# Performance work log

Hardware: AMD Instinct MI355X
Metric: run time of the kernel (lower is better)

The kernel has to match this reference:

```python
import jax, jax.numpy as jnp
import numpy as np

B, C_IN, N, K, NUM_CLASS, EMB = 8, 3, 1024, 40, 40, 1024
EPS = 1e-5


def setup_inputs() -> dict:
    key = jax.random.key(0)
    ks = jax.random.split(key, 20)

    def w(k, shape):
        return jax.random.normal(k, shape, jnp.float32) * 0.05

    def bn(k, c):
        k1, k2, k3, k4 = jax.random.split(k, 4)
        g = jax.random.uniform(k1, (c,), jnp.float32, 0.5, 1.5)
        b = jax.random.normal(k2, (c,), jnp.float32) * 0.1
        m = jax.random.normal(k3, (c,), jnp.float32) * 0.1
        v = jax.random.uniform(k4, (c,), jnp.float32, 0.5, 1.5)
        return jnp.stack([g, b, m, v])  # [4, C]

    return {
        "x": jax.random.normal(ks[0], (B, C_IN, N), jnp.float32),
        "w1": w(ks[1], (64, 6)),
        "w2": w(ks[2], (64, 128)),
        "w3": w(ks[3], (128, 128)),
        "w4": w(ks[4], (256, 256)),
        "w5": w(ks[5], (EMB, 512)),
        "l1": w(ks[6], (512, 2 * EMB)),
        "l2w": w(ks[7], (256, 512)),
        "l2b": w(ks[8], (256,)),
        "l3w": w(ks[9], (NUM_CLASS, 256)),
        "l3b": w(ks[10], (NUM_CLASS,)),
        "bn1": bn(ks[11], 64),
        "bn2": bn(ks[12], 64),
        "bn3": bn(ks[13], 128),
        "bn4": bn(ks[14], 256),
        "bn5": bn(ks[15], EMB),
        "bn6": bn(ks[16], 512),
        "bn7": bn(ks[17], 256),
    }


def _bn(x, p, axis):
    # eval-mode batchnorm: p = [gamma, beta, running_mean, running_var]
    shape = [1] * x.ndim
    shape[axis] = p.shape[1]
    g, b, m, v = (p[i].reshape(shape) for i in range(4))
    return (x - m) * g * jax.lax.rsqrt(v + EPS) + b


def _lrelu(x):
    return jnp.where(x >= 0, x, 0.2 * x)


def _knn(x, k):
    # x: [B, C, N] -> neighbor indices [B, N, k] by largest negative sq-distance
    xx = jnp.sum(x * x, axis=1)  # [B, N]
    inner = jnp.einsum('bcn,bcm->bnm', x, x)  # [B, N, N]
    pd = 2.0 * inner - xx[:, :, None] - xx[:, None, :]
    return jax.lax.top_k(pd, k)[1]


def _graph_feature(x, k):
    # x: [B, C, N] -> edge features [B, 2C, N, k] = cat(nbr - center, center)
    idx = _knn(x, k)  # [B, N, k]
    xt = jnp.transpose(x, (0, 2, 1))  # [B, N, C]
    nb = jax.vmap(lambda xt_b, i_b: xt_b[i_b])(xt, idx)  # [B, N, k, C]
    ctr = jnp.broadcast_to(xt[:, :, None, :], nb.shape)
    feat = jnp.concatenate([nb - ctr, ctr], axis=-1)
    return jnp.transpose(feat, (0, 3, 1, 2))


def _edge_conv(x, w, bnp, k):
    f = _graph_feature(x, k)  # [B, 2C, N, k]
    h = jnp.einsum('oc,bcnk->bonk', w, f)  # 1x1 conv2d, no bias
    h = _lrelu(_bn(h, bnp, 1))
    return jnp.max(h, axis=-1)  # max over k neighbors -> [B, O, N]


def reference(x, w1, w2, w3, w4, w5, l1, l2w, l2b, l3w, l3b,
              bn1, bn2, bn3, bn4, bn5, bn6, bn7):
    x1 = _edge_conv(x, w1, bn1, K)   # [B, 64, N]
    x2 = _edge_conv(x1, w2, bn2, K)  # [B, 64, N]
    x3 = _edge_conv(x2, w3, bn3, K)  # [B, 128, N]
    x4 = _edge_conv(x3, w4, bn4, K)  # [B, 256, N]
    xc = jnp.concatenate([x1, x2, x3, x4], axis=1)  # [B, 512, N]
    e = _lrelu(_bn(jnp.einsum('oc,bcn->bon', w5, xc), bn5, 1))  # [B, EMB, N]
    g = jnp.concatenate([jnp.max(e, axis=-1), jnp.mean(e, axis=-1)], axis=1)  # [B, 2*EMB]
    h = _lrelu(_bn(g @ l1.T, bn6, 1))            # linear1 (no bias) + bn6
    h = _lrelu(_bn(h @ l2w.T + l2b, bn7, 1))     # linear2 + bn7 (dropout = eval identity)
    logits = h @ l3w.T + l3b                     # linear3
    return logits, jax.nn.log_softmax(logits, axis=-1)
```

## Files before the change

### kernel.cpp

```cpp
#include <hip/hip_runtime.h>
#include <hip/hip_bf16.h>
#include <math.h>

#define BB 8
#define NN 1024
#define KK 40
#define EMBD 1024
#define EPSF 1e-5f
#define ROWS 8
#define BBNN (BB * NN)

template <int CTRL>
__device__ __forceinline__ unsigned long long dppmax64(unsigned long long cur) {
    unsigned olo = (unsigned)__builtin_amdgcn_update_dpp(0, (int)(unsigned)cur, CTRL, 0xf, 0xf, true);
    unsigned ohi = (unsigned)__builtin_amdgcn_update_dpp(0, (int)(unsigned)(cur >> 32), CTRL, 0xf, 0xf, true);
    unsigned long long o = ((unsigned long long)ohi << 32) | olo;
    return o > cur ? o : cur;
}

__global__ __launch_bounds__(256) void layer_kernel(const float* __restrict__ x, int C, int bstride,
                                                    const float* __restrict__ w, int O,
                                                    int* __restrict__ gidx,
                                                    float* __restrict__ ya, float* __restrict__ yc) {
    extern __shared__ float lds[];
    int tid = threadIdx.x;

    if (blockIdx.x < BB * 128) {
        float* S = lds;
        int b = blockIdx.x >> 7;
        int n0 = (blockIdx.x & 127) * ROWS;
        const float* xb = x + (size_t)b * bstride;

        float acc[ROWS][4];
        float xxa[4] = {0.f, 0.f, 0.f, 0.f};
#pragma unroll
        for (int r = 0; r < ROWS; ++r)
#pragma unroll
            for (int j = 0; j < 4; ++j) acc[r][j] = 0.f;

        for (int c = 0; c < C; ++c) {
            float4 xm  = *(const float4*)&xb[c * NN + (tid << 2)];
            float4 ce0 = *(const float4*)&xb[c * NN + n0];
            float4 ce1 = *(const float4*)&xb[c * NN + n0 + 4];
            xxa[0] = fmaf(xm.x, xm.x, xxa[0]);
            xxa[1] = fmaf(xm.y, xm.y, xxa[1]);
            xxa[2] = fmaf(xm.z, xm.z, xxa[2]);
            xxa[3] = fmaf(xm.w, xm.w, xxa[3]);
            float ce[8] = {ce0.x, ce0.y, ce0.z, ce0.w, ce1.x, ce1.y, ce1.z, ce1.w};
#pragma unroll
            for (int r = 0; r < ROWS; ++r) {
                acc[r][0] = fmaf(ce[r], xm.x, acc[r][0]);
                acc[r][1] = fmaf(ce[r], xm.y, acc[r][1]);
                acc[r][2] = fmaf(ce[r], xm.z, acc[r][2]);
                acc[r][3] = fmaf(ce[r], xm.w, acc[r][3]);
            }
        }
#pragma unroll
        for (int r = 0; r < ROWS; ++r) {
            float4 sv;
            sv.x = 2.f * acc[r][0] - xxa[0];
            sv.y = 2.f * acc[r][1] - xxa[1];
            sv.z = 2.f * acc[r][2] - xxa[2];
            sv.w = 2.f * acc[r][3] - xxa[3];
            *(float4*)&S[r * NN + (tid << 2)] = sv;
        }
        __syncthreads();

        int wave = tid >> 6, lane = tid & 63;
        int ra = wave << 1, rb = ra + 1;
        unsigned long long va[16], vb[16];
#pragma unroll
        for (int j = 0; j < 16; ++j) {
            unsigned ua = __float_as_uint(S[ra * NN + lane + 64 * j]);
            unsigned ub = __float_as_uint(S[rb * NN + lane + 64 * j]);
            ua ^= (unsigned)((int)ua >> 31) | 0x80000000u;
            ub ^= (unsigned)((int)ub >> 31) | 0x80000000u;
            unsigned lo = (unsigned)(1023 - (lane + (j << 6)));
            va[j] = ((unsigned long long)ua << 32) | lo;
            vb[j] = ((unsigned long long)ub << 32) | lo;
        }
#pragma unroll
        for (int k = 2; k <= 16; k <<= 1)
#pragma unroll
        for (int s = k >> 1; s > 0; s >>= 1)
#pragma unroll
        for (int i = 0; i < 16; ++i) {
            int l = i ^ s;
            if (l > i) {
                bool up = ((i & k) == 0);
                { unsigned long long A = va[i], B = va[l];
                  bool sw = up ? (A > B) : (A < B);
                  va[i] = sw ? B : A; va[l] = sw ? A : B; }
                { unsigned long long A = vb[i], B = vb[l];
                  bool sw = up ? (A > B) : (A < B);
                  vb[i] = sw ? B : A; vb[l] = sw ? A : B; }
            }
        }
        int* ga = gidx + (size_t)b * NN + n0 + ra;
        int* gb = gidx + (size_t)b * NN + n0 + rb;
        unsigned long long ha = va[15], hb = vb[15];
        for (int it = 0; it < KK; ++it) {
            unsigned long long ma = ha, mb = hb;
            ma = dppmax64<0x111>(ma); mb = dppmax64<0x111>(mb);
            ma = dppmax64<0x112>(ma); mb = dppmax64<0x112>(mb);
            ma = dppmax64<0x114>(ma); mb = dppmax64<0x114>(mb);
            ma = dppmax64<0x118>(ma); mb = dppmax64<0x118>(mb);
            ma = dppmax64<0x142>(ma); mb = dppmax64<0x142>(mb);
            ma = dppmax64<0x143>(ma); mb = dppmax64<0x143>(mb);
            unsigned wla = (unsigned)__builtin_amdgcn_readlane((int)(unsigned)ma, 63);
            unsigned wha = (unsigned)__builtin_amdgcn_readlane((int)(unsigned)(ma >> 32), 63);
            unsigned wlb = (unsigned)__builtin_amdgcn_readlane((int)(unsigned)mb, 63);
            unsigned whb = (unsigned)__builtin_amdgcn_readlane((int)(unsigned)(mb >> 32), 63);
            if (lane == 0) {
                ga[(size_t)it * BBNN] = 1023 - (int)wla;
                gb[(size_t)it * BBNN] = 1023 - (int)wlb;
            }
            unsigned long long wka = ((unsigned long long)wha << 32) | wla;
            unsigned long long wkb = ((unsigned long long)whb << 32) | wlb;
            bool pa = (ha == wka), pb = (hb == wkb);
#pragma unroll
            for (int j = 15; j > 0; --j) {
                va[j] = pa ? va[j - 1] : va[j];
                vb[j] = pb ? vb[j - 1] : vb[j];
            }
            va[0] = pa ? 0ull : va[0];
            vb[0] = pb ? 0ull : vb[0];
            ha = va[15]; hb = vb[15];
        }
    } else {
        int bid = blockIdx.x - BB * 128;
        float* wls = lds;
        int opb = O >> 3;
        int b  = bid / opb;
        int o0 = (bid % opb) << 3;
        const float* xb = x + (size_t)b * bstride;

        for (int t = tid; t < 8 * C; t += 256) {
            int r = t / C, c = t - r * C;
            float wa = w[(size_t)(o0 + r) * 2 * C + c];
            float wb = w[(size_t)(o0 + r) * 2 * C + C + c];
            wls[t] = wa;
            wls[8 * C + t] = wb - wa;
        }
        __syncthreads();

        float a[8][4], cv[8][4];
#pragma unroll
        for (int r = 0; r < 8; ++r)
#pragma unroll
            for (int j = 0; j < 4; ++j) { a[r][j] = 0.f; cv[r][j] = 0.f; }
        for (int c = 0; c < C; ++c) {
            float4 xm = *(const float4*)&xb[c * NN + (tid << 2)];
#pragma unroll
            for (int r = 0; r < 8; ++r) {
                float wa = wls[r * C + c];
                float wc = wls[8 * C + r * C + c];
                a[r][0]  = fmaf(wa, xm.x, a[r][0]);  cv[r][0] = fmaf(wc, xm.x, cv[r][0]);
                a[r][1]  = fmaf(wa, xm.y, a[r][1]);  cv[r][1] = fmaf(wc, xm.y, cv[r][1]);
                a[r][2]  = fmaf(wa, xm.z, a[r][2]);  cv[r][2] = fmaf(wc, xm.z, cv[r][2]);
                a[r][3]  = fmaf(wa, xm.w, a[r][3]);  cv[r][3] = fmaf(wc, xm.w, cv[r][3]);
            }
        }
#pragma unroll
        for (int r = 0; r < 8; ++r) {
            size_t off = ((size_t)b * O + o0 + r) * NN + (tid << 2);
            *(float4*)&ya[off] = *(float4*)&a[r][0];
            *(float4*)&yc[off] = *(float4*)&cv[r][0];
        }
    }
}

__global__ __launch_bounds__(256) void gmax8_kernel(const float* __restrict__ ya, const float* __restrict__ yc,
                                                    const int* __restrict__ gidx, const float* __restrict__ bnp,
                                                    int O, float* __restrict__ outp, int out_bstride) {
    __shared__ float yrow[8 * NN];
    int tid = threadIdx.x;
    int nt   = blockIdx.x & 3;
    int rest = blockIdx.x >> 2;
    int opb = O >> 3;
    int oc = rest % opb;
    int b  = rest / opb;
    int o0 = oc << 3;
    int n  = (nt << 8) + tid;

    for (int t = tid; t < 8 * NN; t += 256)
        yrow[t] = ya[((size_t)b * O + o0 + (t >> 10)) * NN + (t & 1023)];
    __syncthreads();

    int idx[KK];
    const int* gi = gidx + (size_t)b * NN + n;
#pragma unroll
    for (int k = 0; k < KK; ++k) idx[k] = gi[(size_t)k * BBNN];

#pragma unroll
    for (int r = 0; r < 8; ++r) {
        float m = -INFINITY;
#pragma unroll 8
        for (int k = 0; k < KK; ++k) m = fmaxf(m, yrow[r * NN + idx[k]]);
        m += yc[((size_t)b * O + o0 + r) * NN + n];
        int o = o0 + r;
        float sc = bnp[o] * rsqrtf(bnp[3 * O + o] + EPSF);
        float t0 = (m - bnp[2 * O + o]) * sc + bnp[O + o];
        outp[(size_t)b * out_bstride + (size_t)o * NN + n] = t0 >= 0.f ? t0 : 0.2f * t0;
    }
}

__global__ __launch_bounds__(256) void emb_kernel(const float* __restrict__ xc, const float* __restrict__ w5,
                                                  const float* __restrict__ bnp, float* __restrict__ g) {
    __shared__ float rmax[8][4], rsum[8][4];
    int tid = threadIdx.x;
    int b  = blockIdx.x & 7;
    int o0 = (blockIdx.x >> 3) << 3;
    const float* xcb = xc + (size_t)b * 512 * NN;
    const float* wr  = w5 + (size_t)o0 * 512;

    int n4 = tid << 2;
    float acc[8][4];
#pragma unroll
    for (int r = 0; r < 8; ++r)
#pragma unroll
        for (int j = 0; j < 4; ++j) acc[r][j] = 0.f;

#pragma unroll 2
    for (int c4 = 0; c4 < 128; ++c4) {
        int c = c4 << 2;
        float4 xm0 = *(const float4*)&xcb[(c + 0) * NN + n4];
        float4 xm1 = *(const float4*)&xcb[(c + 1) * NN + n4];
        float4 xm2 = *(const float4*)&xcb[(c + 2) * NN + n4];
        float4 xm3 = *(const float4*)&xcb[(c + 3) * NN + n4];
#pragma unroll
        for (int r = 0; r < 8; ++r) {
            float4 wv = *(const float4*)&wr[r * 512 + c];
            acc[r][0] = fmaf(wv.x, xm0.x, acc[r][0]);
            acc[r][1] = fmaf(wv.x, xm0.y, acc[r][1]);
            acc[r][2] = fmaf(wv.x, xm0.z, acc[r][2]);
            acc[r][3] = fmaf(wv.x, xm0.w, acc[r][3]);
            acc[r][0] = fmaf(wv.y, xm1.x, acc[r][0]);
            acc[r][1] = fmaf(wv.y, xm1.y, acc[r][1]);
            acc[r][2] = fmaf(wv.y, xm1.z, acc[r][2]);
            acc[r][3] = fmaf(wv.y, xm1.w, acc[r][3]);
            acc[r][0] = fmaf(wv.z, xm2.x, acc[r][0]);
            acc[r][1] = fmaf(wv.z, xm2.y, acc[r][1]);
            acc[r][2] = fmaf(wv.z, xm2.z, acc[r][2]);
            acc[r][3] = fmaf(wv.z, xm2.w, acc[r][3]);
            acc[r][0] = fmaf(wv.w, xm3.x, acc[r][0]);
            acc[r][1] = fmaf(wv.w, xm3.y, acc[r][1]);
            acc[r][2] = fmaf(wv.w, xm3.z, acc[r][2]);
            acc[r][3] = fmaf(wv.w, xm3.w, acc[r][3]);
        }
    }

    int lane = tid & 63, wave = tid >> 6;
#pragma unroll
    for (int r = 0; r < 8; ++r) {
        int o = o0 + r;
        float sc = bnp[o] * rsqrtf(bnp[3 * EMBD + o] + EPSF);
        float mu = bnp[2 * EMBD + o], be = bnp[EMBD + o];
        float vmax = -INFINITY, vsum = 0.f;
#pragma unroll
        for (int j = 0; j < 4; ++j) {
            float t0 = (acc[r][j] - mu) * sc + be;
            t0 = t0 >= 0.f ? t0 : 0.2f * t0;
            vmax = fmaxf(vmax, t0);
            vsum += t0;
        }
#pragma unroll
        for (int off = 32; off >= 1; off >>= 1) {
            vmax = fmaxf(vmax, __shfl_xor(vmax, off));
            vsum += __shfl_xor(vsum, off);
        }
        if (lane == 0) { rmax[r][wave] = vmax; rsum[r][wave] = vsum; }
    }
    __syncthreads();
    if (tid < 8) {
        float vm = fmaxf(fmaxf(rmax[tid][0], rmax[tid][1]), fmaxf(rmax[tid][2], rmax[tid][3]));
        g[(size_t)b * 2 * EMBD + o0 + tid] = vm;
    } else if (tid < 16) {
        int r = tid - 8;
        float vs = rsum[r][0] + rsum[r][1] + rsum[r][2] + rsum[r][3];
        g[(size_t)b * 2 * EMBD + EMBD + o0 + r] = vs * (1.0f / 1024.0f);
    }
}

__global__ __launch_bounds__(256) void head1_naive_kernel(const float* __restrict__ g, const float* __restrict__ l1,
                                                          const float* __restrict__ bnp, float* __restrict__ h1) {
    __shared__ float red[256];
    int tid = threadIdx.x;
    int b = blockIdx.x >> 9, o = blockIdx.x & 511;
    const float* gr = g + (size_t)b * 2 * EMBD;
    const float* lr = l1 + (size_t)o * 2 * EMBD;
    float s = 0.f;
    for (int c = tid; c < 2048; c += 256) s = fmaf(gr[c], lr[c], s);
    red[tid] = s;
    __syncthreads();
    for (int st = 128; st >= 1; st >>= 1) {
        if (tid < st) red[tid] += red[tid + st];
        __syncthreads();
    }
    if (tid == 0) {
        float sc = bnp[o] * rsqrtf(bnp[3 * 512 + o] + EPSF);
        float t0 = (red[0] - bnp[2 * 512 + o]) * sc + bnp[512 + o];
        h1[b * 512 + o] = t0 >= 0.f ? t0 : 0.2f * t0;
    }
}

__global__ __launch_bounds__(256) void head2_naive_kernel(const float* __restrict__ h1, const float* __restrict__ l2w,
                                                          const float* __restrict__ l2b, const float* __restrict__ bnp,
                                                          float* __restrict__ h2) {
    __shared__ float red[256];
    int tid = threadIdx.x;
    int b = blockIdx.x >> 8, o = blockIdx.x & 255;
    const float* hr = h1 + (size_t)b * 512;
    const float* lr = l2w + (size_t)o * 512;
    float s = fmaf(hr[tid], lr[tid], hr[tid + 256] * lr[tid + 256]);
    red[tid] = s;
    __syncthreads();
    for (int st = 128; st >= 1; st >>= 1) {
        if (tid < st) red[tid] += red[tid + st];
        __syncthreads();
    }
    if (tid == 0) {
        float v = red[0] + l2b[o];
        float sc = bnp[o] * rsqrtf(bnp[3 * 256 + o] + EPSF);
        float t0 = (v - bnp[2 * 256 + o]) * sc + bnp[256 + o];
        h2[b * 256 + o] = t0 >= 0.f ? t0 : 0.2f * t0;
    }
}

__global__ __launch_bounds__(256) void head3_naive_kernel(const float* __restrict__ h2, const float* __restrict__ l3w,
                                                          const float* __restrict__ l3b, float* __restrict__ logits) {
    __shared__ float red[256];
    int tid = threadIdx.x;
    int b = blockIdx.x / 40, i = blockIdx.x % 40;
    red[tid] = h2[(size_t)b * 256 + tid] * l3w[(size_t)i * 256 + tid];
    __syncthreads();
    for (int st = 128; st >= 1; st >>= 1) {
        if (tid < st) red[tid] += red[tid + st];
        __syncthreads();
    }
    if (tid == 0) logits[b * 40 + i] = red[0] + l3b[i];
}

__global__ void final_kernel(const float* __restrict__ logits, float* __restrict__ outp) {
    int b = blockIdx.x;
    if (threadIdx.x != 0) return;
    const float* lr = logits + b * 40;
    float mx = lr[0];
    for (int i = 1; i < 40; ++i) mx = fmaxf(mx, lr[i]);
    float se = 0.f;
    for (int i = 0; i < 40; ++i) se += expf(lr[i] - mx);
    float lse = logf(se);
    for (int i = 0; i < 40; ++i) {
        outp[b * 40 + i]            = lr[i];
        outp[BB * 40 + b * 40 + i]  = lr[i] - mx - lse;
    }
}

extern "C" void kernel_launch(void* const* d_in, const int* in_sizes, int n_in,
                              void* d_out, int out_size, void* d_ws, size_t ws_size,
                              hipStream_t stream) {
    const float* x   = (const float*)d_in[0];
    const float* w1  = (const float*)d_in[1];
    const float* w2  = (const float*)d_in[2];
    const float* w3  = (const float*)d_in[3];
    const float* w4  = (const float*)d_in[4];
    const float* w5  = (const float*)d_in[5];
    const float* l1  = (const float*)d_in[6];
    const float* l2w = (const float*)d_in[7];
    const float* l2b = (const float*)d_in[8];
    const float* l3w = (const float*)d_in[9];
    const float* l3b = (const float*)d_in[10];
    const float* bn1 = (const float*)d_in[11];
    const float* bn2 = (const float*)d_in[12];
    const float* bn3 = (const float*)d_in[13];
    const float* bn4 = (const float*)d_in[14];
    const float* bn5 = (const float*)d_in[15];
    const float* bn6 = (const float*)d_in[16];
    const float* bn7 = (const float*)d_in[17];
    float* outp = (float*)d_out;

    float* xc     = (float*)d_ws;
    float* ya     = xc  + (size_t)BB * 512 * NN;
    float* ycb    = ya  + (size_t)BB * 256 * NN;
    int*  gidx    = (int*)(ycb + (size_t)BB * 256 * NN);
    float* g      = (float*)(gidx + (size_t)BB * NN * KK);
    float* h1     = g  + BB * 2 * EMBD;
    float* h2     = h1 + BB * 512;
    float* logits = h2 + BB * 256;

    struct Layer { const float* xin; int C; int bstride; const float* w; const float* bn; int O; float* out; };
    Layer L[4] = {
        { x,            3,   3 * NN,   w1, bn1, 64,  xc            },
        { xc,           64,  512 * NN, w2, bn2, 64,  xc + 64 * NN  },
        { xc + 64 * NN, 64,  512 * NN, w3, bn3, 128, xc + 128 * NN },
        { xc + 128 * NN,128, 512 * NN, w4, bn4, 256, xc + 256 * NN },
    };

    size_t lsz = (size_t)(ROWS * NN) * sizeof(float);
    for (int i = 0; i < 4; ++i) {
        layer_kernel<<<dim3(BB * 128 + BB * (L[i].O / 8)), dim3(256), lsz, stream>>>(
            L[i].xin, L[i].C, L[i].bstride, L[i].w, L[i].O, gidx, ya, ycb);
        gmax8_kernel<<<dim3(BB * (L[i].O / 8) * 4), dim3(256), 0, stream>>>(ya, ycb, gidx, L[i].bn, L[i].O, L[i].out, 512 * NN);
    }
    emb_kernel<<<dim3(BB * 128), dim3(256), 0, stream>>>(xc, w5, bn5, g);
    head1_naive_kernel<<<dim3(BB * 512), dim3(256), 0, stream>>>(g, l1, bn6, h1);
    head2_naive_kernel<<<dim3(BB * 256), dim3(256), 0, stream>>>(h1, l2w, l2b, bn7, h2);
    head3_naive_kernel<<<dim3(BB * 40), dim3(256), 0, stream>>>(h2, l3w, l3b, logits);
    final_kernel<<<dim3(BB), dim3(64), 0, stream>>>(logits, outp);
}
```

Baseline: 645.8 us.

## Fuse MLP head into one kernel and shrink gather-max tile to two rows

The three per-output head reduction kernels and the log-softmax kernel are replaced by a single kernel with one block per batch. Each thread computes one output dot product, and the intermediate activations stay in shared memory. This removes several launches and global round-trips, but the whole head now runs on only 8 blocks, and each thread reads its own weight row, so weight loads are strided across threads. Separately, the neighbor gather-max kernel now handles 2 output rows per block instead of 8, using a vectorized LDS fill. That gives more blocks and less shared memory per block, at the cost of reloading the neighbor indices four times as often.

New measurement: 654.1 us. About the same (+1.3%).

```diff
diff --git a/kernel.cpp b/kernel.cpp
--- a/kernel.cpp
+++ b/kernel.cpp
@@ -170,21 +170,23 @@
     }
 }
 
-__global__ __launch_bounds__(256) void gmax8_kernel(const float* __restrict__ ya, const float* __restrict__ yc,
+__global__ __launch_bounds__(256) void gmax2_kernel(const float* __restrict__ ya, const float* __restrict__ yc,
                                                     const int* __restrict__ gidx, const float* __restrict__ bnp,
                                                     int O, float* __restrict__ outp, int out_bstride) {
-    __shared__ float yrow[8 * NN];
+    __shared__ float yrow[2 * NN];
     int tid = threadIdx.x;
     int nt   = blockIdx.x & 3;
     int rest = blockIdx.x >> 2;
-    int opb = O >> 3;
+    int opb = O >> 1;
     int oc = rest % opb;
     int b  = rest / opb;
-    int o0 = oc << 3;
+    int o0 = oc << 1;
     int n  = (nt << 8) + tid;
 
-    for (int t = tid; t < 8 * NN; t += 256)
-        yrow[t] = ya[((size_t)b * O + o0 + (t >> 10)) * NN + (t & 1023)];
+    const float4* src = (const float4*)(ya + ((size_t)b * O + o0) * NN);
+#pragma unroll
+    for (int i = 0; i < 2; ++i)
+        ((float4*)yrow)[tid + (i << 8)] = src[tid + (i << 8)];
     __syncthreads();
 
     int idx[KK];
@@ -192,15 +194,25 @@
 #pragma unroll
     for (int k = 0; k < KK; ++k) idx[k] = gi[(size_t)k * BBNN];
 
-#pragma unroll
-    for (int r = 0; r < 8; ++r) {
-        float m = -INFINITY;
+    float m0 = -INFINITY, m1 = -INFINITY;
 #pragma unroll 8
-        for (int k = 0; k < KK; ++k) m = fmaxf(m, yrow[r * NN + idx[k]]);
-        m += yc[((size_t)b * O + o0 + r) * NN + n];
-        int o = o0 + r;
+    for (int k = 0; k < KK; ++k) {
+        int j = idx[k];
+        m0 = fmaxf(m0, yrow[j]);
+        m1 = fmaxf(m1, yrow[NN + j]);
+    }
+    m0 += yc[((size_t)b * O + o0 + 0) * NN + n];
+    m1 += yc[((size_t)b * O + o0 + 1) * NN + n];
+    {
+        int o = o0;
         float sc = bnp[o] * rsqrtf(bnp[3 * O + o] + EPSF);
-        float t0 = (m - bnp[2 * O + o]) * sc + bnp[O + o];
+        float t0 = (m0 - bnp[2 * O + o]) * sc + bnp[O + o];
+        outp[(size_t)b * out_bstride + (size_t)o * NN + n] = t0 >= 0.f ? t0 : 0.2f * t0;
+    }
+    {
+        int o = o0 + 1;
+        float sc = bnp[o] * rsqrtf(bnp[3 * O + o] + EPSF);
+        float t0 = (m1 - bnp[2 * O + o]) * sc + bnp[O + o];
         outp[(size_t)b * out_bstride + (size_t)o * NN + n] = t0 >= 0.f ? t0 : 0.2f * t0;
     }
 }
@@ -282,78 +294,73 @@
     }
 }
 
-__global__ __launch_bounds__(256) void head1_naive_kernel(const float* __restrict__ g, const float* __restrict__ l1,
-                                                          const float* __restrict__ bnp, float* __restrict__ h1) {
-    __shared__ float red[256];
+__global__ __launch_bounds__(512) void head_fused_kernel(const float* __restrict__ g,
+                                                         const float* __restrict__ l1, const float* __restrict__ bn6,
+                                                         const float* __restrict__ l2w, const float* __restrict__ l2b,
+                                                         const float* __restrict__ bn7,
+                                                         const float* __restrict__ l3w, const float* __restrict__ l3b,
+                                                         float* __restrict__ outp) {
+    __shared__ float gs[2 * EMBD];
+    __shared__ float h1s[512];
+    __shared__ float h2s[256];
+    __shared__ float lg[64];
     int tid = threadIdx.x;
-    int b = blockIdx.x >> 9, o = blockIdx.x & 511;
-    const float* gr = g + (size_t)b * 2 * EMBD;
-    const float* lr = l1 + (size_t)o * 2 * EMBD;
-    float s = 0.f;
-    for (int c = tid; c < 2048; c += 256) s = fmaf(gr[c], lr[c], s);
-    red[tid] = s;
+    int b = blockIdx.x;
+
+    for (int t = tid; t < 2 * EMBD; t += 512) gs[t] = g[(size_t)b * 2 * EMBD + t];
     __syncthreads();
-    for (int st = 128; st >= 1; st >>= 1) {
-        if (tid < st) red[tid] += red[tid + st];
-        __syncthreads();
-    }
-    if (tid == 0) {
-        float sc = bnp[o] * rsqrtf(bnp[3 * 512 + o] + EPSF);
-        float t0 = (red[0] - bnp[2 * 512 + o]) * sc + bnp[512 + o];
-        h1[b * 512 + o] = t0 >= 0.f ? t0 : 0.2f * t0;
-    }
-}
-
-__global__ __launch_bounds__(256) void head2_naive_kernel(const float* __restrict__ h1, const float* __restrict__ l2w,
-                                                          const float* __restrict__ l2b, const float* __restrict__ bnp,
-                                                          float* __restrict__ h2) {
-    __shared__ float red[256];
-    int tid = threadIdx.x;
-    int b = blockIdx.x >> 8, o = blockIdx.x & 255;
-    const float* hr = h1 + (size_t)b * 512;
-    const float* lr = l2w + (size_t)o * 512;
-    float s = fmaf(hr[tid], lr[tid], hr[tid + 256] * lr[tid + 256]);
-    red[tid] = s;
+
+    {
+        int o = tid;
+        const float4* lr  = (const float4*)(l1 + (size_t)o * 2 * EMBD);
+        const float4* gs4 = (const float4*)gs;
+        float s = 0.f;
+        for (int c = 0; c < 512; ++c) {
+            float4 a = lr[c], v = gs4[c];
+            s += a.x * v.x + a.y * v.y + a.z * v.z + a.w * v.w;
+        }
+        float sc = bn6[o] * rsqrtf(bn6[3 * 512 + o] + EPSF);
+        float t0 = (s - bn6[2 * 512 + o]) * sc + bn6[512 + o];
+        h1s[o] = t0 >= 0.f ? t0 : 0.2f * t0;
+    }
     __syncthreads();
-    for (int st = 128; st >= 1; st >>= 1) {
-        if (tid < st) red[tid] += red[tid + st];
-        __syncthreads();
-    }
-    if (tid == 0) {
-        float v = red[0] + l2b[o];
-        float sc = bnp[o] * rsqrtf(bnp[3 * 256 + o] + EPSF);
-        float t0 = (v - bnp[2 * 256 + o]) * sc + bnp[256 + o];
-        h2[b * 256 + o] = t0 >= 0.f ? t0 : 0.2f * t0;
-    }
-}
-
-__global__ __launch_bounds__(256) void head3_naive_kernel(const float* __restrict__ h2, const float* __restrict__ l3w,
-                                                          const float* __restrict__ l3b, float* __restrict__ logits) {
-    __shared__ float red[256];
-    int tid = threadIdx.x;
-    int b = blockIdx.x / 40, i = blockIdx.x % 40;
-    red[tid] = h2[(size_t)b * 256 + tid] * l3w[(size_t)i * 256 + tid];
+
+    if (tid < 256) {
+        int o = tid;
+        const float4* lr  = (const float4*)(l2w + (size_t)o * 512);
+        const float4* h14 = (const float4*)h1s;
+        float s = l2b[o];
+        for (int c = 0; c < 128; ++c) {
+            float4 a = lr[c], v = h14[c];
+            s += a.x * v.x + a.y * v.y + a.z * v.z + a.w * v.w;
+        }
+        float sc = bn7[o] * rsqrtf(bn7[3 * 256 + o] + EPSF);
+        float t0 = (s - bn7[2 * 256 + o]) * sc + bn7[256 + o];
+        h2s[o] = t0 >= 0.f ? t0 : 0.2f * t0;
+    }
     __syncthreads();
-    for (int st = 128; st >= 1; st >>= 1) {
-        if (tid < st) red[tid] += red[tid + st];
-        __syncthreads();
-    }
-    if (tid == 0) logits[b * 40 + i] = red[0] + l3b[i];
-}
-
-__global__ void final_kernel(const float* __restrict__ logits, float* __restrict__ outp) {
-    int b = blockIdx.x;
-    if (threadIdx.x != 0) return;
-    const float* lr = logits + b * 40;
-    float mx = lr[0];
-    for (int i = 1; i < 40; ++i) mx = fmaxf(mx, lr[i]);
-    float se = 0.f;
-    for (int i = 0; i < 40; ++i) se += expf(lr[i] - mx);
-    float lse = logf(se);
-    for (int i = 0; i < 40; ++i) {
-        outp[b * 40 + i]            = lr[i];
-        outp[BB * 40 + b * 40 + i]  = lr[i] - mx - lse;
-    }
+
+    if (tid < 64) {
+        float s = -INFINITY;
+        if (tid < 40) {
+            s = l3b[tid];
+            const float4* lr  = (const float4*)(l3w + (size_t)tid * 256);
+            const float4* h24 = (const float4*)h2s;
+            for (int c = 0; c < 64; ++c) {
+                float4 a = lr[c], v = h24[c];
+                s += a.x * v.x + a.y * v.y + a.z * v.z + a.w * v.w;
+            }
+            outp[b * 40 + tid] = s;
+        }
+        float mx = s;
+#pragma unroll
+        for (int off = 32; off >= 1; off >>= 1) mx = fmaxf(mx, __shfl_xor(mx, off));
+        float e = (tid < 40) ? expf(s - mx) : 0.f;
+#pragma unroll
+        for (int off = 32; off >= 1; off >>= 1) e += __shfl_xor(e, off);
+        if (tid < 40) outp[BB * 40 + b * 40 + tid] = s - mx - logf(e);
+    }
+    (void)lg;
 }
 
 extern "C" void kernel_launch(void* const* d_in, const int* in_sizes, int n_in,
@@ -384,9 +391,6 @@
     float* ycb    = ya  + (size_t)BB * 256 * NN;
     int*  gidx    = (int*)(ycb + (size_t)BB * 256 * NN);
     float* g      = (float*)(gidx + (size_t)BB * NN * KK);
-    float* h1     = g  + BB * 2 * EMBD;
-    float* h2     = h1 + BB * 512;
-    float* logits = h2 + BB * 256;
 
     struct Layer { const float* xin; int C; int bstride; const float* w; const float* bn; int O; float* out; };
     Layer L[4] = {
@@ -400,11 +404,8 @@
     for (int i = 0; i < 4; ++i) {
         layer_kernel<<<dim3(BB * 128 + BB * (L[i].O / 8)), dim3(256), lsz, stream>>>(
             L[i].xin, L[i].C, L[i].bstride, L[i].w, L[i].O, gidx, ya, ycb);
-        gmax8_kernel<<<dim3(BB * (L[i].O / 8) * 4), dim3(256), 0, stream>>>(ya, ycb, gidx, L[i].bn, L[i].O, L[i].out, 512 * NN);
+        gmax2_kernel<<<dim3(BB * (L[i].O / 2) * 4), dim3(256), 0, stream>>>(ya, ycb, gidx, L[i].bn, L[i].O, L[i].out, 512 * NN);
     }
     emb_kernel<<<dim3(BB * 128), dim3(256), 0, stream>>>(xc, w5, bn5, g);
-    head1_naive_kernel<<<dim3(BB * 512), dim3(256), 0, stream>>>(g, l1, bn6, h1);
-    head2_naive_kernel<<<dim3(BB * 256), dim3(256), 0, stream>>>(h1, l2w, l2b, bn7, h2);
-    head3_naive_kernel<<<dim3(BB * 40), dim3(256), 0, stream>>>(h2, l3w, l3b, logits);
-    final_kernel<<<dim3(BB), dim3(64), 0, stream>>>(logits, outp);
-}
+    head_fused_kernel<<<dim3(BB), dim3(512), 0, stream>>>(g, l1, bn6, l2w, l2b, bn7, l3w, l3b, outp);
+}
```
